# Kernel optimization log

Hardware: AMD Instinct MI355X
Metric: run time of the kernel (lower is better)

## Reference

```python
import jax, jax.numpy as jnp
import numpy as np

HIDDEN = 128
N_NODES = 200000
N_VISITED = 1024


def setup_inputs() -> dict:
    key = jax.random.key(0)
    ks = jax.random.split(key, 7)
    X = jax.random.normal(ks[0], (N_NODES, HIDDEN), dtype=jnp.float32)
    x = jax.random.normal(ks[1], (HIDDEN,), dtype=jnp.float32)
    s = 1.0 / np.sqrt(HIDDEN)
    Wq = jax.random.uniform(ks[2], (3 * HIDDEN, HIDDEN), jnp.float32, -s, s)
    Wk = jax.random.uniform(ks[3], (HIDDEN, HIDDEN), jnp.float32, -s, s)
    Wv = jax.random.uniform(ks[4], (HIDDEN, HIDDEN), jnp.float32, -s, s)
    Wo = jax.random.uniform(ks[5], (HIDDEN, HIDDEN), jnp.float32, -s, s)
    nodes_visited = jax.random.randint(ks[6], (N_VISITED,), 0, N_NODES, dtype=jnp.int32)
    return {
        "X": X, "x": x, "Wq": Wq, "Wk": Wk, "Wv": Wv, "Wo": Wo,
        "nodes_visited": nodes_visited,
        "starting_node": 0, "previous_node": 1,
    }


def reference(X, x, Wq, Wk, Wv, Wo, nodes_visited, starting_node, previous_node):
    # X: [n_nodes, 128]; x: [128]
    n_nodes = X.shape[0]
    # features_concat = [x ; X[start] ; X[prev]]  -> [3*128]
    features_concat = jnp.concatenate([x, X[starting_node], X[previous_node]])
    q = features_concat @ Wq              # [128]
    k = X @ Wk                            # [n_nodes, 128]
    v = X @ Wv                            # [n_nodes, 128]
    u = (k @ q) / jnp.sqrt(jnp.float32(HIDDEN))   # [n_nodes]
    # additive mask: 1 everywhere, 0 at visited nodes (faithful to original)
    mask = jnp.ones((n_nodes,), dtype=X.dtype).at[nodes_visited].set(0.0)
    # final_layer == False branch
    u_ = jax.nn.softmax(u + mask)         # [n_nodes]
    h = u_ @ v                            # [128]
    out = h @ Wo                          # [128]
    return out
```

## Files before the change

kernel.cpp:

```cpp
#include <hip/hip_runtime.h>
#include <math.h>

#define HIDDEN 128
#define MAIN_BLOCKS 512
#define MAIN_THREADS 1024
#define MAX_BMAP_WORDS 6272

__global__ __launch_bounds__(512) void prep_kernel(
    const float* __restrict__ X, const float* __restrict__ x,
    const float* __restrict__ Wq, const float* __restrict__ Wk,
    const int* __restrict__ startp, const int* __restrict__ prevp,
    float* __restrict__ qk)
{
    __shared__ float fc[384];
    __shared__ float qpart[4][HIDDEN];
    __shared__ float qv[HIDDEN];
    const int t   = threadIdx.x;
    const int col = t & (HIDDEN - 1);
    const int seg = t >> 7;

    if (t < 128)       fc[t]       = x[t];
    else if (t < 256)  fc[t]       = X[(size_t)startp[0] * HIDDEN + (t - 128)];
    else if (t < 384)  fc[t]       = X[(size_t)prevp[0]  * HIDDEN + (t - 256)];
    __syncthreads();

    float acc = 0.f;
    const int m0 = seg * 96;
    #pragma unroll 8
    for (int m = 0; m < 96; ++m)
        acc += fc[m0 + m] * Wq[(size_t)(m0 + m) * HIDDEN + col];
    qpart[seg][col] = acc;
    __syncthreads();
    if (t < HIDDEN)
        qv[t] = qpart[0][t] + qpart[1][t] + qpart[2][t] + qpart[3][t];
    __syncthreads();

    const int hw  = t >> 5;
    const int sub = t & 31;
    const float4 qv4 = *(const float4*)(&qv[sub << 2]);
    for (int row = hw; row < HIDDEN; row += 16) {
        const float4 wk4 = *(const float4*)(Wk + (size_t)row * HIDDEN + (sub << 2));
        float p = wk4.x * qv4.x + wk4.y * qv4.y + wk4.z * qv4.z + wk4.w * qv4.w;
        #pragma unroll
        for (int off = 16; off >= 1; off >>= 1)
            p += __shfl_xor(p, off, 64);
        if (sub == 0) qk[row] = p * 0.08838834764831845f;
    }
}

__global__ __launch_bounds__(MAIN_THREADS) void main_kernel(
    const float* __restrict__ X, const int* __restrict__ visited, int nv,
    const float* __restrict__ qk,
    float* __restrict__ Mb, float* __restrict__ Sb, float* __restrict__ Gb,
    int n)
{
    __shared__ unsigned bmap[MAX_BMAP_WORDS];
    __shared__ float m_arr[32];
    __shared__ float s_arr[32];
    __shared__ float g_all[32 * HIDDEN];

    const int tid  = threadIdx.x;
    const int lane = tid & 63;
    const int sub  = lane & 31;
    const int half = (lane >> 5) & 1;
    const int wavesPerBlock = blockDim.x >> 6;
    const int gw  = blockIdx.x * wavesPerBlock + (tid >> 6);
    const int vhw = gw * 2 + half;
    const int T   = gridDim.x * wavesPerBlock * 2;

    const int nwords = (n + 31) >> 5;
    for (int w = tid; w < nwords; w += blockDim.x) bmap[w] = 0u;
    __syncthreads();
    for (int i = tid; i < nv; i += blockDim.x) {
        const int v = visited[i];
        atomicOr(&bmap[v >> 5], 1u << (v & 31));
    }
    __syncthreads();

    const float4 qkv = *(const float4*)(qk + (sub << 2));

    float m = -INFINITY, s = 0.f;
    float g0 = 0.f, g1 = 0.f, g2 = 0.f, g3 = 0.f;

    for (int r = vhw; r < n; r += T) {
        const float4 xv = *(const float4*)(X + (size_t)r * HIDDEN + (sub << 2));
        float p = xv.x * qkv.x + xv.y * qkv.y + xv.z * qkv.z + xv.w * qkv.w;
        #pragma unroll
        for (int off = 16; off >= 1; off >>= 1)
            p += __shfl_xor(p, off, 64);
        const float maskv = ((bmap[r >> 5] >> (r & 31)) & 1u) ? 0.f : 1.f;
        const float u = p + maskv;
        const float mn    = fmaxf(m, u);
        const float scale = __expf(m - mn);
        const float w     = __expf(u - mn);
        s  = s  * scale + w;
        g0 = g0 * scale + w * xv.x;
        g1 = g1 * scale + w * xv.y;
        g2 = g2 * scale + w * xv.z;
        g3 = g3 * scale + w * xv.w;
        m  = mn;
    }

    const int hw = tid >> 5;
    *(float4*)(&g_all[hw * HIDDEN + (sub << 2)]) = make_float4(g0, g1, g2, g3);
    if (sub == 0) { m_arr[hw] = m; s_arr[hw] = s; }
    __syncthreads();

    float mb = m_arr[0];
    #pragma unroll
    for (int h = 1; h < 32; ++h) mb = fmaxf(mb, m_arr[h]);

    if (tid < HIDDEN) {
        float G = 0.f;
        #pragma unroll 4
        for (int h = 0; h < 32; ++h)
            G += g_all[h * HIDDEN + tid] * __expf(m_arr[h] - mb);
        Gb[blockIdx.x * HIDDEN + tid] = G;
    } else if (tid == HIDDEN) {
        float S = 0.f;
        #pragma unroll
        for (int h = 0; h < 32; ++h) S += s_arr[h] * __expf(m_arr[h] - mb);
        Sb[blockIdx.x] = S;
        Mb[blockIdx.x] = mb;
    }
}

__global__ __launch_bounds__(512) void finish_kernel(
    const float* __restrict__ Mb, const float* __restrict__ Sb,
    const float* __restrict__ Gb,
    const float* __restrict__ Wv, const float* __restrict__ Wo,
    float* __restrict__ out, int B)
{
    __shared__ float red[512];
    __shared__ float e[MAIN_BLOCKS];
    __shared__ float part[4][HIDDEN];
    __shared__ float pvec[HIDDEN];
    __shared__ float hvec[HIDDEN];
    const int t   = threadIdx.x;
    const int col = t & (HIDDEN - 1);
    const int seg = t >> 7;

    const float mt = (t < B) ? Mb[t] : -INFINITY;
    red[t] = mt; __syncthreads();
    for (int st = 256; st >= 1; st >>= 1) {
        if (t < st) red[t] = fmaxf(red[t], red[t + st]);
        __syncthreads();
    }
    const float M = red[0];
    __syncthreads();

    float ls = 0.f;
    if (t < B) { const float eb = __expf(mt - M); e[t] = eb; ls = Sb[t] * eb; }
    red[t] = ls; __syncthreads();
    for (int st = 256; st >= 1; st >>= 1) {
        if (t < st) red[t] += red[t + st];
        __syncthreads();
    }
    const float S = red[0];
    __syncthreads();

    {
        float acc = 0.f;
        const int b0 = seg * (B >> 2);
        #pragma unroll 8
        for (int b = 0; b < (MAIN_BLOCKS >> 2); ++b)
            acc += Gb[(size_t)(b0 + b) * HIDDEN + col] * e[b0 + b];
        part[seg][col] = acc;
    }
    __syncthreads();
    if (t < HIDDEN)
        pvec[t] = (part[0][t] + part[1][t] + part[2][t] + part[3][t]) / S;
    __syncthreads();

    {
        float acc = 0.f;
        const int m0 = seg * 32;
        #pragma unroll 8
        for (int m = 0; m < 32; ++m)
            acc += pvec[m0 + m] * Wv[(size_t)(m0 + m) * HIDDEN + col];
        part[seg][col] = acc;
    }
    __syncthreads();
    if (t < HIDDEN)
        hvec[t] = part[0][t] + part[1][t] + part[2][t] + part[3][t];
    __syncthreads();

    {
        float acc = 0.f;
        const int m0 = seg * 32;
        #pragma unroll 8
        for (int m = 0; m < 32; ++m)
            acc += hvec[m0 + m] * Wo[(size_t)(m0 + m) * HIDDEN + col];
        part[seg][col] = acc;
    }
    __syncthreads();
    if (t < HIDDEN)
        out[t] = part[0][t] + part[1][t] + part[2][t] + part[3][t];
}

extern "C" void kernel_launch(void* const* d_in, const int* in_sizes, int n_in,
                              void* d_out, int out_size, void* d_ws, size_t ws_size,
                              hipStream_t stream)
{
    const float* X       = (const float*)d_in[0];
    const float* x       = (const float*)d_in[1];
    const float* Wq      = (const float*)d_in[2];
    const float* Wk      = (const float*)d_in[3];
    const float* Wv      = (const float*)d_in[4];
    const float* Wo      = (const float*)d_in[5];
    const int*   visited = (const int*)d_in[6];
    const int*   startp  = (const int*)d_in[7];
    const int*   prevp   = (const int*)d_in[8];

    const int n  = in_sizes[0] / HIDDEN;
    const int nv = in_sizes[6];

    float* ws = (float*)d_ws;
    float* qk = ws;
    float* Mb = ws + 128;
    float* Sb = Mb + MAIN_BLOCKS;
    float* Gb = Sb + MAIN_BLOCKS;

    prep_kernel<<<1, 512, 0, stream>>>(X, x, Wq, Wk, startp, prevp, qk);
    main_kernel<<<MAIN_BLOCKS, MAIN_THREADS, 0, stream>>>(X, visited, nv, qk, Mb, Sb, Gb, n);
    finish_kernel<<<1, 512, 0, stream>>>(Mb, Sb, Gb, Wv, Wo, (float*)d_out, MAIN_BLOCKS);
}
```

Measured before the change: 188.9 us.

## Fuse query/key projection prep into main streaming kernel, computing qk per block

The single-block prep kernel is removed. Every block of the main kernel now recomputes the query projection and the Wk product into shared memory, overlapping that work with the visited-bitmap build. This drops one kernel launch and the serial dependency on a one-block kernel. In exchange, all 512 blocks redundantly read Wq and Wk (small, likely cached) and use more shared memory per block.

```diff
diff --git a/kernel.cpp b/kernel.cpp
--- a/kernel.cpp
+++ b/kernel.cpp
@@ -6,55 +6,19 @@
 #define MAIN_THREADS 1024
 #define MAX_BMAP_WORDS 6272
 
-__global__ __launch_bounds__(512) void prep_kernel(
+__global__ __launch_bounds__(MAIN_THREADS) void fused_kernel(
     const float* __restrict__ X, const float* __restrict__ x,
     const float* __restrict__ Wq, const float* __restrict__ Wk,
+    const int* __restrict__ visited, int nv,
     const int* __restrict__ startp, const int* __restrict__ prevp,
-    float* __restrict__ qk)
-{
-    __shared__ float fc[384];
-    __shared__ float qpart[4][HIDDEN];
-    __shared__ float qv[HIDDEN];
-    const int t   = threadIdx.x;
-    const int col = t & (HIDDEN - 1);
-    const int seg = t >> 7;
-
-    if (t < 128)       fc[t]       = x[t];
-    else if (t < 256)  fc[t]       = X[(size_t)startp[0] * HIDDEN + (t - 128)];
-    else if (t < 384)  fc[t]       = X[(size_t)prevp[0]  * HIDDEN + (t - 256)];
-    __syncthreads();
-
-    float acc = 0.f;
-    const int m0 = seg * 96;
-    #pragma unroll 8
-    for (int m = 0; m < 96; ++m)
-        acc += fc[m0 + m] * Wq[(size_t)(m0 + m) * HIDDEN + col];
-    qpart[seg][col] = acc;
-    __syncthreads();
-    if (t < HIDDEN)
-        qv[t] = qpart[0][t] + qpart[1][t] + qpart[2][t] + qpart[3][t];
-    __syncthreads();
-
-    const int hw  = t >> 5;
-    const int sub = t & 31;
-    const float4 qv4 = *(const float4*)(&qv[sub << 2]);
-    for (int row = hw; row < HIDDEN; row += 16) {
-        const float4 wk4 = *(const float4*)(Wk + (size_t)row * HIDDEN + (sub << 2));
-        float p = wk4.x * qv4.x + wk4.y * qv4.y + wk4.z * qv4.z + wk4.w * qv4.w;
-        #pragma unroll
-        for (int off = 16; off >= 1; off >>= 1)
-            p += __shfl_xor(p, off, 64);
-        if (sub == 0) qk[row] = p * 0.08838834764831845f;
-    }
-}
-
-__global__ __launch_bounds__(MAIN_THREADS) void main_kernel(
-    const float* __restrict__ X, const int* __restrict__ visited, int nv,
-    const float* __restrict__ qk,
     float* __restrict__ Mb, float* __restrict__ Sb, float* __restrict__ Gb,
     int n)
 {
     __shared__ unsigned bmap[MAX_BMAP_WORDS];
+    __shared__ float fc[384];
+    __shared__ float qpart[8][HIDDEN];
+    __shared__ float qv[HIDDEN];
+    __shared__ float qks[HIDDEN];
     __shared__ float m_arr[32];
     __shared__ float s_arr[32];
     __shared__ float g_all[32 * HIDDEN];
@@ -63,21 +27,60 @@
     const int lane = tid & 63;
     const int sub  = lane & 31;
     const int half = (lane >> 5) & 1;
-    const int wavesPerBlock = blockDim.x >> 6;
+
+    const int nwords = (n + 31) >> 5;
+    float fcv = 0.f;
+    if (tid < 384) {
+        if (tid < 128)      fcv = x[tid];
+        else if (tid < 256) fcv = X[(size_t)startp[0] * HIDDEN + (tid - 128)];
+        else                fcv = X[(size_t)prevp[0]  * HIDDEN + (tid - 256)];
+    }
+    for (int w = tid; w < nwords; w += MAIN_THREADS) bmap[w] = 0u;
+    if (tid < 384) fc[tid] = fcv;
+    __syncthreads();
+
+    for (int i = tid; i < nv; i += MAIN_THREADS) {
+        const int v = visited[i];
+        atomicOr(&bmap[v >> 5], 1u << (v & 31));
+    }
+    {
+        const int col = tid & (HIDDEN - 1);
+        const int seg = tid >> 7;
+        const int m0  = seg * 48;
+        float acc = 0.f;
+        #pragma unroll 8
+        for (int m = 0; m < 48; ++m)
+            acc += fc[m0 + m] * Wq[(size_t)(m0 + m) * HIDDEN + col];
+        qpart[seg][col] = acc;
+    }
+    __syncthreads();
+    if (tid < HIDDEN)
+        qv[tid] = ((qpart[0][tid] + qpart[1][tid]) + (qpart[2][tid] + qpart[3][tid]))
+                + ((qpart[4][tid] + qpart[5][tid]) + (qpart[6][tid] + qpart[7][tid]));
+    __syncthreads();
+
+    {
+        const int hw0 = tid >> 5;
+        const float4 qv4 = *(const float4*)(&qv[sub << 2]);
+        #pragma unroll
+        for (int k = 0; k < 4; ++k) {
+            const int row = hw0 + (k << 5);
+            const float4 wk4 = *(const float4*)(Wk + (size_t)row * HIDDEN + (sub << 2));
+            float p = wk4.x * qv4.x + wk4.y * qv4.y + wk4.z * qv4.z + wk4.w * qv4.w;
+            #pragma unroll
+            for (int off = 16; off >= 1; off >>= 1)
+                p += __shfl_xor(p, off, 64);
+            if (sub == 0) qks[row] = p * 0.08838834764831845f;
+        }
+    }
+    __syncthreads();
+
+    const int wavesPerBlock = MAIN_THREADS >> 6;
     const int gw  = blockIdx.x * wavesPerBlock + (tid >> 6);
     const int vhw = gw * 2 + half;
     const int T   = gridDim.x * wavesPerBlock * 2;
 
-    const int nwords = (n + 31) >> 5;
-    for (int w = tid; w < nwords; w += blockDim.x) bmap[w] = 0u;
-    __syncthreads();
-    for (int i = tid; i < nv; i += blockDim.x) {
-        const int v = visited[i];
-        atomicOr(&bmap[v >> 5], 1u << (v & 31));
-    }
-    __syncthreads();
-
-    const float4 qkv = *(const float4*)(qk + (sub << 2));
+    const float4 qkv = *(const float4*)(&qks[sub << 2]);
 
     float m = -INFINITY, s = 0.f;
     float g0 = 0.f, g1 = 0.f, g2 = 0.f, g3 = 0.f;
@@ -89,7 +92,7 @@
         for (int off = 16; off >= 1; off >>= 1)
             p += __shfl_xor(p, off, 64);
         const float maskv = ((bmap[r >> 5] >> (r & 31)) & 1u) ? 0.f : 1.f;
-        const float u = p + maskv;
+        const float u  = p + maskv;
         const float mn    = fmaxf(m, u);
         const float scale = __expf(m - mn);
         const float w     = __expf(u - mn);
@@ -216,12 +219,11 @@
     const int nv = in_sizes[6];
 
     float* ws = (float*)d_ws;
-    float* qk = ws;
     float* Mb = ws + 128;
     float* Sb = Mb + MAIN_BLOCKS;
     float* Gb = Sb + MAIN_BLOCKS;
 
-    prep_kernel<<<1, 512, 0, stream>>>(X, x, Wq, Wk, startp, prevp, qk);
-    main_kernel<<<MAIN_BLOCKS, MAIN_THREADS, 0, stream>>>(X, visited, nv, qk, Mb, Sb, Gb, n);
+    fused_kernel<<<MAIN_BLOCKS, MAIN_THREADS, 0, stream>>>(
+        X, x, Wq, Wk, visited, nv, startp, prevp, Mb, Sb, Gb, n);
     finish_kernel<<<1, 512, 0, stream>>>(Mb, Sb, Gb, Wv, Wo, (float*)d_out, MAIN_BLOCKS);
 }
```

Result: faster. 180.7 us (-4.3%).
